# Optimization experiments

Measured on AMD Instinct MI355X. Metric: run time of the kernel, lower is better.

Reference implementation:

```python
import jax, jax.numpy as jnp
import numpy as np

E_PROP = 0.8
DT = 0.02
AX = 0.2   # dt / tau_x = 0.02 / 0.1
AW = 0.02  # dt / tau_w = 0.02 / 1.0


def _ei_mask(out_size, in_size, e_prop, zero_prop, remove_diag):
    """EILinear mask: +1 for excitatory cols, -1 inhibitory, 0 for zeroed cols/diag."""
    e = int(e_prop * in_size)
    sign = np.ones(in_size, np.float32)
    sign[e:] = -1.0
    zc = int(round(zero_prop * in_size))
    exist = np.ones(in_size, np.float32)
    if zc > 0:
        exist[in_size - zc:] = 0.0
    m = np.tile((sign * exist)[None, :], (out_size, 1))
    if remove_diag:
        assert out_size == in_size
        m[np.eye(out_size, dtype=bool)] = 0.0
    return jnp.asarray(m)


def setup_inputs() -> dict:
    T, B, I, H, O = 32, 16, 128, 384, 32
    key = jax.random.key(0)
    ks = jax.random.split(key, 10)
    u = lambda k, s, hi: jax.random.uniform(k, s, jnp.float32, 0.0, hi)
    s_in = (1.0 / I) ** 0.5
    s_h = (1.0 / H) ** 0.5
    s_hz = (1.0 / (H - round((1.0 - E_PROP) * H))) ** 0.5  # zero_cols removed from fan-in
    return {
        "x": jax.random.normal(ks[0], (T, B, I), jnp.float32),
        "Rs": jax.random.uniform(ks[1], (T, B, 1), jnp.float32),
        "W_x2c": u(ks[2], (H, I), 0.5 * s_in),
        "W_c2c": u(ks[3], (H, H), s_h),
        "b_c2c": jnp.zeros((H,), jnp.float32),
        "W_c2h": u(ks[4], (H, H), 0.5 * s_hz),
        "W_h2h": u(ks[5], (H, H), s_h),
        "b_h2h": jnp.zeros((H,), jnp.float32),
        "W_h2o": u(ks[6], (O, H), 0.5 * s_hz),
        "W_attn": u(ks[7], (H, H), 0.1 * s_hz),
        "b_attn": jnp.zeros((H,), jnp.float32),
        "kappa": jnp.full((12,), AW, jnp.float32),
    }


def reference(x, Rs, W_x2c, W_c2c, b_c2c, W_c2h, W_h2h, b_h2h, W_h2o, W_attn, b_attn, kappa):
    T, B, I = x.shape
    H = W_c2c.shape[0]
    O = W_h2o.shape[0]
    retanh = lambda z: jnp.tanh(jax.nn.relu(z))

    m_x2c = _ei_mask(H, I, 1.0, 0.0, False)
    m_c2c = _ei_mask(H, H, E_PROP, 0.0, True)
    m_c2h = _ei_mask(H, H, 1.0, 1.0 - E_PROP, False)
    m_h2h = _ei_mask(H, H, E_PROP, 0.0, True)
    m_h2o = _ei_mask(O, H, 1.0, 1.0 - E_PROP, False)
    m_attn = _ei_mask(H, H, E_PROP, 1.0 - E_PROP, False)

    def plin(W, mask, w_fast, inp, bias=None):
        # (relu(W) + w_fast) * mask, per-batch matmul: [B,O,I] @ [B,I] -> [B,O]
        eff = (jax.nn.relu(W)[None] + w_fast) * mask[None]
        out = jnp.einsum('boi,bi->bo', eff, inp)
        return out if bias is None else out + bias

    def lin(W, mask, inp, bias=None):
        out = inp @ (jax.nn.relu(W) * mask).T
        return out if bias is None else out + bias

    def plast(w, R, pre, post, k, W_slow):
        # w: [B,O,I]; R: [B,1,1]; pre: [B,I]; post: [B,O]
        new_w = (w * (1.0 - AW)
                 + DT * R * (k[0] * pre[:, None, :]
                             + k[1] * post[:, :, None]
                             + k[2] * post[:, :, None] * pre[:, None, :]))
        lb = -jax.lax.stop_gradient(jax.nn.relu(W_slow))[None]
        return jnp.maximum(new_w, lb)

    def step(carry, inputs):
        x_t, R_t = inputs  # [B,I], [B,1]
        sc, oc, sh, oh, wxc, wcc, wch, whh = carry
        attn = retanh(lin(W_attn, m_attn, oh, b_attn))  # attention_type == 'bias'
        tic = plin(W_x2c, m_x2c, wxc, x_t) + plin(W_c2c, m_c2c, wcc, oc, b_c2c) + attn
        nsc = sc * (1.0 - AX) + tic * AX
        noc = retanh(nsc)
        tih = plin(W_c2h, m_c2h, wch, noc) + plin(W_h2h, m_h2h, whh, oh, b_h2h)
        nsh = sh * (1.0 - AX) + tih * AX
        noh = retanh(nsh)
        R = R_t[:, :, None]  # [B,1,1]
        wxc2 = plast(wxc, R, x_t, noc, kappa[0:3], W_x2c)
        wcc2 = plast(wcc, R, oc, noc, kappa[3:6], W_c2c)
        wch2 = plast(wch, R, noc, noh, kappa[6:9], W_c2h)
        whh2 = plast(whh, R, oh, noh, kappa[9:12], W_h2h)
        out_t = lin(W_h2o, m_h2o, noh)
        return (nsc, noc, nsh, noh, wxc2, wcc2, wch2, whh2), out_t

    z = jnp.zeros((B, H), x.dtype)
    carry0 = (z, z, z, z,
              jnp.zeros((B, H, I), x.dtype),
              jnp.zeros((B, H, H), x.dtype),
              jnp.zeros((B, H, H), x.dtype),
              jnp.zeros((B, H, H), x.dtype))
    _, outs = jax.lax.scan(step, carry0, (x, Rs))
    return outs  # [T, B, O]
```

## Files before the change

### kernel.cpp

```cpp
#include <hip/hip_runtime.h>


#define NT 32
#define NBATCH 16
#define DI 128
#define DH 384
#define DOUT 32
#define CSZ (NT * NBATCH * DH)

__device__ __forceinline__ float retanh_f(float z) {
  z = fmaxf(z, 0.0f);
  float e = __expf(-2.0f * z);
  return (1.0f - e) / (1.0f + e);
}

__device__ __forceinline__ float aldf(const float* p) {
  return __hip_atomic_load(p, __ATOMIC_RELAXED, __HIP_MEMORY_SCOPE_AGENT);
}
__device__ __forceinline__ void pubG(float* p, float v) {
  __hip_atomic_store(p, v, __ATOMIC_RELAXED, __HIP_MEMORY_SCOPE_AGENT);
}

__device__ __forceinline__ void gather6G(const float* src, int lane, float arr[6]) {
  const float* p = src + lane;
  float v0, v1, v2, v3, v4, v5;
  for (;;) {
    v0 = aldf(p + 0 * 64);
    v1 = aldf(p + 1 * 64);
    v2 = aldf(p + 2 * 64);
    v3 = aldf(p + 3 * 64);
    v4 = aldf(p + 4 * 64);
    v5 = aldf(p + 5 * 64);
    const bool ok = (v0 != 0.f) & (v1 != 0.f) & (v2 != 0.f) &
                    (v3 != 0.f) & (v4 != 0.f) & (v5 != 0.f);
    if (ok) break;
  }
  arr[0] = v0 - 2.f; arr[1] = v1 - 2.f; arr[2] = v2 - 2.f;
  arr[3] = v3 - 2.f; arr[4] = v4 - 2.f; arr[5] = v5 - 2.f;
}

__global__ __launch_bounds__(512, 2) void hrnn(
    const float* __restrict__ x, const float* __restrict__ Rs,
    const float* __restrict__ Wx, const float* __restrict__ Wc, const float* __restrict__ bc,
    const float* __restrict__ Wch, const float* __restrict__ Whh, const float* __restrict__ bh,
    const float* __restrict__ Wo, const float* __restrict__ Wa, const float* __restrict__ ba,
    const float* __restrict__ kap, float* __restrict__ out, float* __restrict__ comm) {
  const int tid  = threadIdx.x;
  const int lane = tid & 63;
  const int wv   = tid >> 6;
  const int bid  = blockIdx.x;
  const int b = ((bid & 7) << 1) | ((bid >> 3) & 1);
  const int k = bid >> 4;

  float* noc_buf = comm;
  float* noh_buf = comm + CSZ;

  __shared__ float sh_noh[DH];
  __shared__ float sh_noc[DH];

  const int og0 = k * 24 + wv * 3;
  const bool do_out = (k == 15);

  float wxc[3][2], wcc[3][6], wchv[3][5], whh[3][6];
  float rWx[3][2], rWc[3][6], rWch[3][5], rWhh[3][6], rWa[3][5];
  float sc[3], shs[3], bcr[3], bar[3], bhr[3];
  float ohr[6], ocr[6];
  float rWo[4][5];

#pragma unroll
  for (int r = 0; r < 3; ++r) {
    const int og = og0 + r;
#pragma unroll
    for (int j = 0; j < 2; ++j) { rWx[r][j] = fmaxf(Wx[og*DI + j*64 + lane], 0.f); wxc[r][j] = 0.f; }
#pragma unroll
    for (int j = 0; j < 6; ++j) { rWc[r][j] = fmaxf(Wc[og*DH + j*64 + lane], 0.f); wcc[r][j] = 0.f; }
#pragma unroll
    for (int j = 0; j < 5; ++j) { rWch[r][j] = fmaxf(Wch[og*DH + j*64 + lane], 0.f); wchv[r][j] = 0.f; }
#pragma unroll
    for (int j = 0; j < 6; ++j) { rWhh[r][j] = fmaxf(Whh[og*DH + j*64 + lane], 0.f); whh[r][j] = 0.f; }
#pragma unroll
    for (int j = 0; j < 5; ++j) {
      float w = fmaxf(Wa[og*DH + j*64 + lane], 0.f);
      rWa[r][j] = (j == 4 && lane >= 51) ? 0.f : w;
    }
    sc[r] = 0.f; shs[r] = 0.f;
    bcr[r] = bc[og]; bar[r] = ba[og]; bhr[r] = bh[og];
  }
  if (do_out) {
#pragma unroll
    for (int m = 0; m < 4; ++m) {
      const int o = wv * 4 + m;
#pragma unroll
      for (int j = 0; j < 5; ++j) {
        float w = fmaxf(Wo[o*DH + j*64 + lane], 0.f);
        rWo[m][j] = (j == 4 && lane >= 51) ? 0.f : w;
      }
    }
  }
#pragma unroll
  for (int j = 0; j < 6; ++j) { ohr[j] = 0.f; ocr[j] = 0.f; }
  float kp[12];
#pragma unroll
  for (int j = 0; j < 12; ++j) kp[j] = kap[j];

  float xp0 = x[b*DI + lane];
  float xp1 = x[b*DI + 64 + lane];
  float dtRp = 0.02f * Rs[b];

  for (int t = 0; t < NT; ++t) {
    const int toff = t * NBATCH * DH + b * DH;

    if (t > 0) {
      if (wv == 0) {
        float tmp[6];
        gather6G(noh_buf + toff - NBATCH * DH, lane, tmp);
#pragma unroll
        for (int j = 0; j < 6; ++j) sh_noh[j * 64 + lane] = tmp[j];
      }
      __syncthreads();
#pragma unroll
      for (int j = 0; j < 6; ++j) ohr[j] = sh_noh[j * 64 + lane];
    }

    const float dtR = dtRp;
    const float x0 = xp0;
    const float x1 = xp1;
    const float oh4s = (lane < 51) ? ohr[4] : -ohr[4];
    const float oc4s = (lane < 51) ? ocr[4] : -ocr[4];
    const float inC[6] = { ocr[0], ocr[1], ocr[2], ocr[3], oc4s, -ocr[5] };

    float nocr[3];
#pragma unroll
    for (int r = 0; r < 3; ++r) {
      const int og = og0 + r;
      const int dj = og >> 6, dl = og & 63;
      float accA = 0.f, accT = 0.f;
#pragma unroll
      for (int j = 0; j < 5; ++j) accA += rWa[r][j] * ohr[j];
      accT += (rWx[r][0] + wxc[r][0]) * x0;
      accT += (rWx[r][1] + wxc[r][1]) * x1;
#pragma unroll
      for (int j = 0; j < 6; ++j) {
        float term = (rWc[r][j] + wcc[r][j]) * inC[j];
        if (j == dj) term = (lane == dl) ? 0.f : term;
        accT += term;
      }
#pragma unroll
      for (int mm = 1; mm <= 32; mm <<= 1) {
        accA += __shfl_xor(accA, mm, 64);
        accT += __shfl_xor(accT, mm, 64);
      }
      const float attn = retanh_f(accA + bar[r]);
      const float tic = accT + bcr[r] + attn;
      sc[r] = 0.8f*sc[r] + 0.2f*tic;
      nocr[r] = retanh_f(sc[r]);
    }
    {
      float mine = (lane == 0) ? nocr[0] : (lane == 1) ? nocr[1] : nocr[2];
      if (lane < 3) pubG(noc_buf + toff + og0 + lane, mine + 2.0f);
    }

    if (t < NT-1) {
      xp0 = x[((t+1)*NBATCH + b)*DI + lane];
      xp1 = x[((t+1)*NBATCH + b)*DI + 64 + lane];
      dtRp = 0.02f * Rs[(t+1)*NBATCH + b];
    }
    if (do_out && t > 0) {
#pragma unroll
      for (int m = 0; m < 4; ++m) {
        float a = 0.f;
#pragma unroll
        for (int j = 0; j < 5; ++j) a += rWo[m][j] * ohr[j];
#pragma unroll
        for (int mm = 1; mm <= 32; mm <<= 1) a += __shfl_xor(a, mm, 64);
        if (lane == 0) out[(t-1)*NBATCH*DOUT + b*DOUT + wv*4 + m] = a;
      }
    }
    if (t < NT-1) {
      float axc[2], bxc[2];
#pragma unroll
      for (int j = 0; j < 2; ++j) {
        const float pre = (j == 0) ? x0 : x1;
        axc[j] = dtR*kp[0]*pre; bxc[j] = dtR*(kp[1] + kp[2]*pre);
      }
      float acc_[6], bcc_[6];
#pragma unroll
      for (int j = 0; j < 6; ++j) { acc_[j] = dtR*kp[3]*ocr[j]; bcc_[j] = dtR*(kp[4] + kp[5]*ocr[j]); }
#pragma unroll
      for (int r = 0; r < 3; ++r) {
        const float post = nocr[r];
#pragma unroll
        for (int j = 0; j < 2; ++j)
          wxc[r][j] = fmaxf(fmaf(wxc[r][j], 0.98f, fmaf(bxc[j], post, axc[j])), -rWx[r][j]);
#pragma unroll
        for (int j = 0; j < 6; ++j)
          wcc[r][j] = fmaxf(fmaf(wcc[r][j], 0.98f, fmaf(bcc_[j], post, acc_[j])), -rWc[r][j]);
      }
    }

    if (wv == 0) {
      float tmp[6];
      gather6G(noc_buf + toff, lane, tmp);
#pragma unroll
      for (int j = 0; j < 6; ++j) sh_noc[j * 64 + lane] = tmp[j];
    }
    __syncthreads();
    float ncr[6];
#pragma unroll
    for (int j = 0; j < 6; ++j) ncr[j] = sh_noc[j * 64 + lane];

    const float nc4z = (lane < 51) ? ncr[4] : 0.f;
    const float inH[6] = { ohr[0], ohr[1], ohr[2], ohr[3], oh4s, -ohr[5] };
    const float inN[5] = { ncr[0], ncr[1], ncr[2], ncr[3], nc4z };
    float nohr[3];
#pragma unroll
    for (int r = 0; r < 3; ++r) {
      const int og = og0 + r;
      const int dj = og >> 6, dl = og & 63;
      float acc = 0.f;
#pragma unroll
      for (int j = 0; j < 5; ++j) acc += (rWch[r][j] + wchv[r][j]) * inN[j];
#pragma unroll
      for (int j = 0; j < 6; ++j) {
        float term = (rWhh[r][j] + whh[r][j]) * inH[j];
        if (j == dj) term = (lane == dl) ? 0.f : term;
        acc += term;
      }
#pragma unroll
      for (int mm = 1; mm <= 32; mm <<= 1) acc += __shfl_xor(acc, mm, 64);
      const float tih = acc + bhr[r];
      shs[r] = 0.8f*shs[r] + 0.2f*tih;
      nohr[r] = retanh_f(shs[r]);
    }
    {
      float mine = (lane == 0) ? nohr[0] : (lane == 1) ? nohr[1] : nohr[2];
      if (lane < 3) pubG(noh_buf + toff + og0 + lane, mine + 2.0f);
    }

    if (t < NT-1) {
      float an_[5], bn_[5];
#pragma unroll
      for (int j = 0; j < 5; ++j) { an_[j] = dtR*kp[6]*ncr[j]; bn_[j] = dtR*(kp[7] + kp[8]*ncr[j]); }
      float ah_[6], bh_[6];
#pragma unroll
      for (int j = 0; j < 6; ++j) { ah_[j] = dtR*kp[9]*ohr[j]; bh_[j] = dtR*(kp[10] + kp[11]*ohr[j]); }
#pragma unroll
      for (int r = 0; r < 3; ++r) {
        const float post = nohr[r];
#pragma unroll
        for (int j = 0; j < 5; ++j)
          wchv[r][j] = fmaxf(fmaf(wchv[r][j], 0.98f, fmaf(bn_[j], post, an_[j])), -rWch[r][j]);
#pragma unroll
        for (int j = 0; j < 6; ++j)
          whh[r][j] = fmaxf(fmaf(whh[r][j], 0.98f, fmaf(bh_[j], post, ah_[j])), -rWhh[r][j]);
      }
    }
#pragma unroll
    for (int j = 0; j < 6; ++j) ocr[j] = ncr[j];
  }

  if (do_out) {
    if (wv == 0) {
      float tmp[6];
      gather6G(noh_buf + (NT-1)*NBATCH*DH + b*DH, lane, tmp);
#pragma unroll
      for (int j = 0; j < 6; ++j) sh_noh[j * 64 + lane] = tmp[j];
    }
    __syncthreads();
    float oh2[6];
#pragma unroll
    for (int j = 0; j < 6; ++j) oh2[j] = sh_noh[j * 64 + lane];
#pragma unroll
    for (int m = 0; m < 4; ++m) {
      float a = 0.f;
#pragma unroll
      for (int j = 0; j < 5; ++j) a += rWo[m][j] * oh2[j];
#pragma unroll
      for (int mm = 1; mm <= 32; mm <<= 1) a += __shfl_xor(a, mm, 64);
      if (lane == 0) out[(NT-1)*NBATCH*DOUT + b*DOUT + wv*4 + m] = a;
    }
  }
}

extern "C" void kernel_launch(void* const* d_in, const int* in_sizes, int n_in,
                              void* d_out, int out_size, void* d_ws, size_t ws_size,
                              hipStream_t stream) {
  const float* x   = (const float*)d_in[0];
  const float* Rs  = (const float*)d_in[1];
  const float* Wx  = (const float*)d_in[2];
  const float* Wc  = (const float*)d_in[3];
  const float* bc  = (const float*)d_in[4];
  const float* Wch = (const float*)d_in[5];
  const float* Whh = (const float*)d_in[6];
  const float* bh  = (const float*)d_in[7];
  const float* Wo  = (const float*)d_in[8];
  const float* Wa  = (const float*)d_in[9];
  const float* ba  = (const float*)d_in[10];
  const float* kap = (const float*)d_in[11];
  float* out = (float*)d_out;

  float* comm = (float*)d_ws;
  hipMemsetAsync(comm, 0, (size_t)2 * CSZ * sizeof(float), stream);

  hipLaunchKernelGGL(hrnn, dim3(256), dim3(512), 0, stream,
                     x, Rs, Wx, Wc, bc, Wch, Whh, bh, Wo, Wa, ba, kap,
                     out, comm);
}
```

Before: 170.0 us.

## Split compute and polling waves, with dedicated poller waves filling shared state

Each block of 8 waves now has 6 compute waves handling 4 rows each, plus two dedicated waves that poll the cross-block noc and noh buffers and fill shared memory. Before, the compute waves did this themselves. The aim is to overlap the global spin-gather with the compute waves' plasticity updates and to keep polling off the compute waves' critical path. Output-projection weights are no longer held in registers; they are reloaded from global memory each step, which lowers register pressure at the cost of extra loads. Each compute wave now carries more register state, and the block still synchronises twice per step.

```diff
diff --git a/kernel.cpp b/kernel.cpp
--- a/kernel.cpp
+++ b/kernel.cpp
@@ -58,226 +58,225 @@
   __shared__ float sh_noh[DH];
   __shared__ float sh_noc[DH];
 
-  const int og0 = k * 24 + wv * 3;
-  const bool do_out = (k == 15);
-
-  float wxc[3][2], wcc[3][6], wchv[3][5], whh[3][6];
-  float rWx[3][2], rWc[3][6], rWch[3][5], rWhh[3][6], rWa[3][5];
-  float sc[3], shs[3], bcr[3], bar[3], bhr[3];
+  const bool is_cw    = (wv < 6);
+  const bool is_pollC = (wv == 6);
+  const bool is_pollH = (wv == 7);
+  const int  og0 = k * 24 + wv * 4;
+  const bool do_out = (k == 15) && is_cw;
+
+  float wxc[4][2], wcc[4][6], wchv[4][5], whh[4][6];
+  float rWx[4][2], rWc[4][6], rWch[4][5], rWhh[4][6], rWa[4][5];
+  float sc[4], shs[4], bcr[4], bar4[4], bhr[4];
   float ohr[6], ocr[6];
-  float rWo[4][5];
-
-#pragma unroll
-  for (int r = 0; r < 3; ++r) {
-    const int og = og0 + r;
-#pragma unroll
-    for (int j = 0; j < 2; ++j) { rWx[r][j] = fmaxf(Wx[og*DI + j*64 + lane], 0.f); wxc[r][j] = 0.f; }
-#pragma unroll
-    for (int j = 0; j < 6; ++j) { rWc[r][j] = fmaxf(Wc[og*DH + j*64 + lane], 0.f); wcc[r][j] = 0.f; }
-#pragma unroll
-    for (int j = 0; j < 5; ++j) { rWch[r][j] = fmaxf(Wch[og*DH + j*64 + lane], 0.f); wchv[r][j] = 0.f; }
-#pragma unroll
-    for (int j = 0; j < 6; ++j) { rWhh[r][j] = fmaxf(Whh[og*DH + j*64 + lane], 0.f); whh[r][j] = 0.f; }
-#pragma unroll
-    for (int j = 0; j < 5; ++j) {
-      float w = fmaxf(Wa[og*DH + j*64 + lane], 0.f);
-      rWa[r][j] = (j == 4 && lane >= 51) ? 0.f : w;
+  float kp[12];
+  float xp0 = 0.f, xp1 = 0.f, dtRp = 0.f;
+
+  if (is_cw) {
+#pragma unroll
+    for (int r = 0; r < 4; ++r) {
+      const int og = og0 + r;
+#pragma unroll
+      for (int j = 0; j < 2; ++j) { rWx[r][j] = fmaxf(Wx[og*DI + j*64 + lane], 0.f); wxc[r][j] = 0.f; }
+#pragma unroll
+      for (int j = 0; j < 6; ++j) { rWc[r][j] = fmaxf(Wc[og*DH + j*64 + lane], 0.f); wcc[r][j] = 0.f; }
+#pragma unroll
+      for (int j = 0; j < 5; ++j) { rWch[r][j] = fmaxf(Wch[og*DH + j*64 + lane], 0.f); wchv[r][j] = 0.f; }
+#pragma unroll
+      for (int j = 0; j < 6; ++j) { rWhh[r][j] = fmaxf(Whh[og*DH + j*64 + lane], 0.f); whh[r][j] = 0.f; }
+#pragma unroll
+      for (int j = 0; j < 5; ++j) {
+        float w = fmaxf(Wa[og*DH + j*64 + lane], 0.f);
+        rWa[r][j] = (j == 4 && lane >= 51) ? 0.f : w;
+      }
+      sc[r] = 0.f; shs[r] = 0.f;
+      bcr[r] = bc[og]; bar4[r] = ba[og]; bhr[r] = bh[og];
     }
-    sc[r] = 0.f; shs[r] = 0.f;
-    bcr[r] = bc[og]; bar[r] = ba[og]; bhr[r] = bh[og];
+#pragma unroll
+    for (int j = 0; j < 12; ++j) kp[j] = kap[j];
+    xp0 = x[b*DI + lane];
+    xp1 = x[b*DI + 64 + lane];
+    dtRp = 0.02f * Rs[b];
   }
-  if (do_out) {
-#pragma unroll
-    for (int m = 0; m < 4; ++m) {
-      const int o = wv * 4 + m;
-#pragma unroll
-      for (int j = 0; j < 5; ++j) {
-        float w = fmaxf(Wo[o*DH + j*64 + lane], 0.f);
-        rWo[m][j] = (j == 4 && lane >= 51) ? 0.f : w;
-      }
+#pragma unroll
+  for (int j = 0; j < 6; ++j) { ohr[j] = 0.f; ocr[j] = 0.f; }
+
+  for (int t = 0; t < NT; ++t) {
+    const int toff = t * NBATCH * DH + b * DH;
+
+    __syncthreads();
+    if (is_cw) {
+      if (t > 0) {
+#pragma unroll
+        for (int j = 0; j < 6; ++j) ohr[j] = sh_noh[j * 64 + lane];
+      }
+      const float dtR = dtRp;
+      const float x0 = xp0;
+      const float x1 = xp1;
+      const float oc4s = (lane < 51) ? ocr[4] : -ocr[4];
+      const float inC[6] = { ocr[0], ocr[1], ocr[2], ocr[3], oc4s, -ocr[5] };
+      float nocr[4];
+#pragma unroll
+      for (int r = 0; r < 4; ++r) {
+        const int og = og0 + r;
+        const int dj = og >> 6, dl = og & 63;
+        float accA = 0.f, accT = 0.f;
+#pragma unroll
+        for (int j = 0; j < 5; ++j) accA += rWa[r][j] * ohr[j];
+        accT += (rWx[r][0] + wxc[r][0]) * x0;
+        accT += (rWx[r][1] + wxc[r][1]) * x1;
+#pragma unroll
+        for (int j = 0; j < 6; ++j) {
+          float term = (rWc[r][j] + wcc[r][j]) * inC[j];
+          if (j == dj) term = (lane == dl) ? 0.f : term;
+          accT += term;
+        }
+#pragma unroll
+        for (int mm = 1; mm <= 32; mm <<= 1) {
+          accA += __shfl_xor(accA, mm, 64);
+          accT += __shfl_xor(accT, mm, 64);
+        }
+        const float attn = retanh_f(accA + bar4[r]);
+        const float tic = accT + bcr[r] + attn;
+        sc[r] = 0.8f*sc[r] + 0.2f*tic;
+        nocr[r] = retanh_f(sc[r]);
+      }
+      {
+        float mine = (lane == 0) ? nocr[0] : (lane == 1) ? nocr[1]
+                   : (lane == 2) ? nocr[2] : nocr[3];
+        if (lane < 4) pubG(noc_buf + toff + og0 + lane, mine + 2.0f);
+      }
+      if (t < NT-1) {
+        float axc[2], bxc[2];
+#pragma unroll
+        for (int j = 0; j < 2; ++j) {
+          const float pre = (j == 0) ? x0 : x1;
+          axc[j] = dtR*kp[0]*pre; bxc[j] = dtR*(kp[1] + kp[2]*pre);
+        }
+        float acc_[6], bcc_[6];
+#pragma unroll
+        for (int j = 0; j < 6; ++j) { acc_[j] = dtR*kp[3]*ocr[j]; bcc_[j] = dtR*(kp[4] + kp[5]*ocr[j]); }
+#pragma unroll
+        for (int r = 0; r < 4; ++r) {
+          const float post = nocr[r];
+#pragma unroll
+          for (int j = 0; j < 2; ++j)
+            wxc[r][j] = fmaxf(fmaf(wxc[r][j], 0.98f, fmaf(bxc[j], post, axc[j])), -rWx[r][j]);
+#pragma unroll
+          for (int j = 0; j < 6; ++j)
+            wcc[r][j] = fmaxf(fmaf(wcc[r][j], 0.98f, fmaf(bcc_[j], post, acc_[j])), -rWc[r][j]);
+        }
+      }
+      if (do_out && t > 0) {
+#pragma unroll
+        for (int m = 0; m < 6; ++m) {
+          const int row = wv + 6 * m;
+          if (row < DOUT) {
+            float a = 0.f;
+#pragma unroll
+            for (int j = 0; j < 5; ++j) {
+              float w = fmaxf(Wo[row*DH + j*64 + lane], 0.f);
+              if (j == 4 && lane >= 51) w = 0.f;
+              a += w * ohr[j];
+            }
+#pragma unroll
+            for (int mm = 1; mm <= 32; mm <<= 1) a += __shfl_xor(a, mm, 64);
+            if (lane == 0) out[(t-1)*NBATCH*DOUT + b*DOUT + row] = a;
+          }
+        }
+      }
+    } else if (is_pollC) {
+      float tmp[6];
+      gather6G(noc_buf + toff, lane, tmp);
+#pragma unroll
+      for (int j = 0; j < 6; ++j) sh_noc[j * 64 + lane] = tmp[j];
+    }
+
+    __syncthreads();
+    if (is_cw) {
+      float ncr[6];
+#pragma unroll
+      for (int j = 0; j < 6; ++j) ncr[j] = sh_noc[j * 64 + lane];
+      const float dtR = dtRp;
+      const float nc4z = (lane < 51) ? ncr[4] : 0.f;
+      const float oh4s = (lane < 51) ? ohr[4] : -ohr[4];
+      const float inH[6] = { ohr[0], ohr[1], ohr[2], ohr[3], oh4s, -ohr[5] };
+      const float inN[5] = { ncr[0], ncr[1], ncr[2], ncr[3], nc4z };
+      float nohr[4];
+#pragma unroll
+      for (int r = 0; r < 4; ++r) {
+        const int og = og0 + r;
+        const int dj = og >> 6, dl = og & 63;
+        float acc = 0.f;
+#pragma unroll
+        for (int j = 0; j < 5; ++j) acc += (rWch[r][j] + wchv[r][j]) * inN[j];
+#pragma unroll
+        for (int j = 0; j < 6; ++j) {
+          float term = (rWhh[r][j] + whh[r][j]) * inH[j];
+          if (j == dj) term = (lane == dl) ? 0.f : term;
+          acc += term;
+        }
+#pragma unroll
+        for (int mm = 1; mm <= 32; mm <<= 1) acc += __shfl_xor(acc, mm, 64);
+        const float tih = acc + bhr[r];
+        shs[r] = 0.8f*shs[r] + 0.2f*tih;
+        nohr[r] = retanh_f(shs[r]);
+      }
+      {
+        float mine = (lane == 0) ? nohr[0] : (lane == 1) ? nohr[1]
+                   : (lane == 2) ? nohr[2] : nohr[3];
+        if (lane < 4) pubG(noh_buf + toff + og0 + lane, mine + 2.0f);
+      }
+      if (t < NT-1) {
+        float an_[5], bn_[5];
+#pragma unroll
+        for (int j = 0; j < 5; ++j) { an_[j] = dtR*kp[6]*ncr[j]; bn_[j] = dtR*(kp[7] + kp[8]*ncr[j]); }
+        float ah_[6], bh_[6];
+#pragma unroll
+        for (int j = 0; j < 6; ++j) { ah_[j] = dtR*kp[9]*ohr[j]; bh_[j] = dtR*(kp[10] + kp[11]*ohr[j]); }
+#pragma unroll
+        for (int r = 0; r < 4; ++r) {
+          const float post = nohr[r];
+#pragma unroll
+          for (int j = 0; j < 5; ++j)
+            wchv[r][j] = fmaxf(fmaf(wchv[r][j], 0.98f, fmaf(bn_[j], post, an_[j])), -rWch[r][j]);
+#pragma unroll
+          for (int j = 0; j < 6; ++j)
+            whh[r][j] = fmaxf(fmaf(whh[r][j], 0.98f, fmaf(bh_[j], post, ah_[j])), -rWhh[r][j]);
+        }
+        xp0 = x[((t+1)*NBATCH + b)*DI + lane];
+        xp1 = x[((t+1)*NBATCH + b)*DI + 64 + lane];
+        dtRp = 0.02f * Rs[(t+1)*NBATCH + b];
+      }
+#pragma unroll
+      for (int j = 0; j < 6; ++j) ocr[j] = ncr[j];
+    } else if (is_pollH) {
+      float tmp[6];
+      gather6G(noh_buf + toff, lane, tmp);
+#pragma unroll
+      for (int j = 0; j < 6; ++j) sh_noh[j * 64 + lane] = tmp[j];
     }
   }
-#pragma unroll
-  for (int j = 0; j < 6; ++j) { ohr[j] = 0.f; ocr[j] = 0.f; }
-  float kp[12];
-#pragma unroll
-  for (int j = 0; j < 12; ++j) kp[j] = kap[j];
-
-  float xp0 = x[b*DI + lane];
-  float xp1 = x[b*DI + 64 + lane];
-  float dtRp = 0.02f * Rs[b];
-
-  for (int t = 0; t < NT; ++t) {
-    const int toff = t * NBATCH * DH + b * DH;
-
-    if (t > 0) {
-      if (wv == 0) {
-        float tmp[6];
-        gather6G(noh_buf + toff - NBATCH * DH, lane, tmp);
-#pragma unroll
-        for (int j = 0; j < 6; ++j) sh_noh[j * 64 + lane] = tmp[j];
-      }
-      __syncthreads();
-#pragma unroll
-      for (int j = 0; j < 6; ++j) ohr[j] = sh_noh[j * 64 + lane];
-    }
-
-    const float dtR = dtRp;
-    const float x0 = xp0;
-    const float x1 = xp1;
-    const float oh4s = (lane < 51) ? ohr[4] : -ohr[4];
-    const float oc4s = (lane < 51) ? ocr[4] : -ocr[4];
-    const float inC[6] = { ocr[0], ocr[1], ocr[2], ocr[3], oc4s, -ocr[5] };
-
-    float nocr[3];
-#pragma unroll
-    for (int r = 0; r < 3; ++r) {
-      const int og = og0 + r;
-      const int dj = og >> 6, dl = og & 63;
-      float accA = 0.f, accT = 0.f;
-#pragma unroll
-      for (int j = 0; j < 5; ++j) accA += rWa[r][j] * ohr[j];
-      accT += (rWx[r][0] + wxc[r][0]) * x0;
-      accT += (rWx[r][1] + wxc[r][1]) * x1;
-#pragma unroll
-      for (int j = 0; j < 6; ++j) {
-        float term = (rWc[r][j] + wcc[r][j]) * inC[j];
-        if (j == dj) term = (lane == dl) ? 0.f : term;
-        accT += term;
-      }
-#pragma unroll
-      for (int mm = 1; mm <= 32; mm <<= 1) {
-        accA += __shfl_xor(accA, mm, 64);
-        accT += __shfl_xor(accT, mm, 64);
-      }
-      const float attn = retanh_f(accA + bar[r]);
-      const float tic = accT + bcr[r] + attn;
-      sc[r] = 0.8f*sc[r] + 0.2f*tic;
-      nocr[r] = retanh_f(sc[r]);
-    }
-    {
-      float mine = (lane == 0) ? nocr[0] : (lane == 1) ? nocr[1] : nocr[2];
-      if (lane < 3) pubG(noc_buf + toff + og0 + lane, mine + 2.0f);
-    }
-
-    if (t < NT-1) {
-      xp0 = x[((t+1)*NBATCH + b)*DI + lane];
-      xp1 = x[((t+1)*NBATCH + b)*DI + 64 + lane];
-      dtRp = 0.02f * Rs[(t+1)*NBATCH + b];
-    }
-    if (do_out && t > 0) {
-#pragma unroll
-      for (int m = 0; m < 4; ++m) {
+
+  __syncthreads();
+  if (do_out) {
+    float oh2[6];
+#pragma unroll
+    for (int j = 0; j < 6; ++j) oh2[j] = sh_noh[j * 64 + lane];
+#pragma unroll
+    for (int m = 0; m < 6; ++m) {
+      const int row = wv + 6 * m;
+      if (row < DOUT) {
         float a = 0.f;
 #pragma unroll
-        for (int j = 0; j < 5; ++j) a += rWo[m][j] * ohr[j];
+        for (int j = 0; j < 5; ++j) {
+          float w = fmaxf(Wo[row*DH + j*64 + lane], 0.f);
+          if (j == 4 && lane >= 51) w = 0.f;
+          a += w * oh2[j];
+        }
 #pragma unroll
         for (int mm = 1; mm <= 32; mm <<= 1) a += __shfl_xor(a, mm, 64);
-        if (lane == 0) out[(t-1)*NBATCH*DOUT + b*DOUT + wv*4 + m] = a;
-      }
-    }
-    if (t < NT-1) {
-      float axc[2], bxc[2];
-#pragma unroll
-      for (int j = 0; j < 2; ++j) {
-        const float pre = (j == 0) ? x0 : x1;
-        axc[j] = dtR*kp[0]*pre; bxc[j] = dtR*(kp[1] + kp[2]*pre);
-      }
-      float acc_[6], bcc_[6];
-#pragma unroll
-      for (int j = 0; j < 6; ++j) { acc_[j] = dtR*kp[3]*ocr[j]; bcc_[j] = dtR*(kp[4] + kp[5]*ocr[j]); }
-#pragma unroll
-      for (int r = 0; r < 3; ++r) {
-        const float post = nocr[r];
-#pragma unroll
-        for (int j = 0; j < 2; ++j)
-          wxc[r][j] = fmaxf(fmaf(wxc[r][j], 0.98f, fmaf(bxc[j], post, axc[j])), -rWx[r][j]);
-#pragma unroll
-        for (int j = 0; j < 6; ++j)
-          wcc[r][j] = fmaxf(fmaf(wcc[r][j], 0.98f, fmaf(bcc_[j], post, acc_[j])), -rWc[r][j]);
-      }
-    }
-
-    if (wv == 0) {
-      float tmp[6];
-      gather6G(noc_buf + toff, lane, tmp);
-#pragma unroll
-      for (int j = 0; j < 6; ++j) sh_noc[j * 64 + lane] = tmp[j];
-    }
-    __syncthreads();
-    float ncr[6];
-#pragma unroll
-    for (int j = 0; j < 6; ++j) ncr[j] = sh_noc[j * 64 + lane];
-
-    const float nc4z = (lane < 51) ? ncr[4] : 0.f;
-    const float inH[6] = { ohr[0], ohr[1], ohr[2], ohr[3], oh4s, -ohr[5] };
-    const float inN[5] = { ncr[0], ncr[1], ncr[2], ncr[3], nc4z };
-    float nohr[3];
-#pragma unroll
-    for (int r = 0; r < 3; ++r) {
-      const int og = og0 + r;
-      const int dj = og >> 6, dl = og & 63;
-      float acc = 0.f;
-#pragma unroll
-      for (int j = 0; j < 5; ++j) acc += (rWch[r][j] + wchv[r][j]) * inN[j];
-#pragma unroll
-      for (int j = 0; j < 6; ++j) {
-        float term = (rWhh[r][j] + whh[r][j]) * inH[j];
-        if (j == dj) term = (lane == dl) ? 0.f : term;
-        acc += term;
-      }
-#pragma unroll
-      for (int mm = 1; mm <= 32; mm <<= 1) acc += __shfl_xor(acc, mm, 64);
-      const float tih = acc + bhr[r];
-      shs[r] = 0.8f*shs[r] + 0.2f*tih;
-      nohr[r] = retanh_f(shs[r]);
-    }
-    {
-      float mine = (lane == 0) ? nohr[0] : (lane == 1) ? nohr[1] : nohr[2];
-      if (lane < 3) pubG(noh_buf + toff + og0 + lane, mine + 2.0f);
-    }
-
-    if (t < NT-1) {
-      float an_[5], bn_[5];
-#pragma unroll
-      for (int j = 0; j < 5; ++j) { an_[j] = dtR*kp[6]*ncr[j]; bn_[j] = dtR*(kp[7] + kp[8]*ncr[j]); }
-      float ah_[6], bh_[6];
-#pragma unroll
-      for (int j = 0; j < 6; ++j) { ah_[j] = dtR*kp[9]*ohr[j]; bh_[j] = dtR*(kp[10] + kp[11]*ohr[j]); }
-#pragma unroll
-      for (int r = 0; r < 3; ++r) {
-        const float post = nohr[r];
-#pragma unroll
-        for (int j = 0; j < 5; ++j)
-          wchv[r][j] = fmaxf(fmaf(wchv[r][j], 0.98f, fmaf(bn_[j], post, an_[j])), -rWch[r][j]);
-#pragma unroll
-        for (int j = 0; j < 6; ++j)
-          whh[r][j] = fmaxf(fmaf(whh[r][j], 0.98f, fmaf(bh_[j], post, ah_[j])), -rWhh[r][j]);
-      }
-    }
-#pragma unroll
-    for (int j = 0; j < 6; ++j) ocr[j] = ncr[j];
-  }
-
-  if (do_out) {
-    if (wv == 0) {
-      float tmp[6];
-      gather6G(noh_buf + (NT-1)*NBATCH*DH + b*DH, lane, tmp);
-#pragma unroll
-      for (int j = 0; j < 6; ++j) sh_noh[j * 64 + lane] = tmp[j];
-    }
-    __syncthreads();
-    float oh2[6];
-#pragma unroll
-    for (int j = 0; j < 6; ++j) oh2[j] = sh_noh[j * 64 + lane];
-#pragma unroll
-    for (int m = 0; m < 4; ++m) {
-      float a = 0.f;
-#pragma unroll
-      for (int j = 0; j < 5; ++j) a += rWo[m][j] * oh2[j];
-#pragma unroll
-      for (int mm = 1; mm <= 32; mm <<= 1) a += __shfl_xor(a, mm, 64);
-      if (lane == 0) out[(NT-1)*NBATCH*DOUT + b*DOUT + wv*4 + m] = a;
+        if (lane == 0) out[(NT-1)*NBATCH*DOUT + b*DOUT + row] = a;
+      }
     }
   }
 }
```

After: 391.9 us. 2.31x slower.

## Add dedicated polling wavefronts so compute waves skip cross-block gather

Applied to the files above, without the earlier changes.

Grows each block from 8 to 10 wavefronts. Two new wavefronts do nothing but spin on the global noc and noh exchange buffers and stage the results into shared memory. Compute wavefronts no longer run the gather themselves, and the loop is rearranged so the noh poll for the next step runs while the compute waves finish the plasticity updates. This costs more threads per block and a changed launch bound (640, 3), which may constrain register allocation. The extra spinning wave per phase also consumes issue slots.

```diff
diff --git a/kernel.cpp b/kernel.cpp
--- a/kernel.cpp
+++ b/kernel.cpp
@@ -39,7 +39,7 @@
   arr[3] = v3 - 2.f; arr[4] = v4 - 2.f; arr[5] = v5 - 2.f;
 }
 
-__global__ __launch_bounds__(512, 2) void hrnn(
+__global__ __launch_bounds__(640, 3) void hrnn(
     const float* __restrict__ x, const float* __restrict__ Rs,
     const float* __restrict__ Wx, const float* __restrict__ Wc, const float* __restrict__ bc,
     const float* __restrict__ Wch, const float* __restrict__ Whh, const float* __restrict__ bh,
@@ -58,33 +58,45 @@
   __shared__ float sh_noh[DH];
   __shared__ float sh_noc[DH];
 
-  const int og0 = k * 24 + wv * 3;
-  const bool do_out = (k == 15);
+  const bool is_cw    = (wv < 8);
+  const bool is_pollC = (wv == 8);
+  const bool is_pollH = (wv == 9);
+  const int  og0 = k * 24 + wv * 3;
+  const bool do_out = (k == 15) && is_cw;
 
   float wxc[3][2], wcc[3][6], wchv[3][5], whh[3][6];
   float rWx[3][2], rWc[3][6], rWch[3][5], rWhh[3][6], rWa[3][5];
-  float sc[3], shs[3], bcr[3], bar[3], bhr[3];
+  float sc[3], shs[3], bcr[3], bar3[3], bhr[3];
   float ohr[6], ocr[6];
   float rWo[4][5];
-
-#pragma unroll
-  for (int r = 0; r < 3; ++r) {
-    const int og = og0 + r;
-#pragma unroll
-    for (int j = 0; j < 2; ++j) { rWx[r][j] = fmaxf(Wx[og*DI + j*64 + lane], 0.f); wxc[r][j] = 0.f; }
-#pragma unroll
-    for (int j = 0; j < 6; ++j) { rWc[r][j] = fmaxf(Wc[og*DH + j*64 + lane], 0.f); wcc[r][j] = 0.f; }
-#pragma unroll
-    for (int j = 0; j < 5; ++j) { rWch[r][j] = fmaxf(Wch[og*DH + j*64 + lane], 0.f); wchv[r][j] = 0.f; }
-#pragma unroll
-    for (int j = 0; j < 6; ++j) { rWhh[r][j] = fmaxf(Whh[og*DH + j*64 + lane], 0.f); whh[r][j] = 0.f; }
-#pragma unroll
-    for (int j = 0; j < 5; ++j) {
-      float w = fmaxf(Wa[og*DH + j*64 + lane], 0.f);
-      rWa[r][j] = (j == 4 && lane >= 51) ? 0.f : w;
-    }
-    sc[r] = 0.f; shs[r] = 0.f;
-    bcr[r] = bc[og]; bar[r] = ba[og]; bhr[r] = bh[og];
+  float kp[12];
+  float xp0 = 0.f, xp1 = 0.f, dtRp = 0.f;
+
+  if (is_cw) {
+#pragma unroll
+    for (int r = 0; r < 3; ++r) {
+      const int og = og0 + r;
+#pragma unroll
+      for (int j = 0; j < 2; ++j) { rWx[r][j] = fmaxf(Wx[og*DI + j*64 + lane], 0.f); wxc[r][j] = 0.f; }
+#pragma unroll
+      for (int j = 0; j < 6; ++j) { rWc[r][j] = fmaxf(Wc[og*DH + j*64 + lane], 0.f); wcc[r][j] = 0.f; }
+#pragma unroll
+      for (int j = 0; j < 5; ++j) { rWch[r][j] = fmaxf(Wch[og*DH + j*64 + lane], 0.f); wchv[r][j] = 0.f; }
+#pragma unroll
+      for (int j = 0; j < 6; ++j) { rWhh[r][j] = fmaxf(Whh[og*DH + j*64 + lane], 0.f); whh[r][j] = 0.f; }
+#pragma unroll
+      for (int j = 0; j < 5; ++j) {
+        float w = fmaxf(Wa[og*DH + j*64 + lane], 0.f);
+        rWa[r][j] = (j == 4 && lane >= 51) ? 0.f : w;
+      }
+      sc[r] = 0.f; shs[r] = 0.f;
+      bcr[r] = bc[og]; bar3[r] = ba[og]; bhr[r] = bh[og];
+    }
+#pragma unroll
+    for (int j = 0; j < 12; ++j) kp[j] = kap[j];
+    xp0 = x[b*DI + lane];
+    xp1 = x[b*DI + 64 + lane];
+    dtRp = 0.02f * Rs[b];
   }
   if (do_out) {
 #pragma unroll
@@ -99,174 +111,157 @@
   }
 #pragma unroll
   for (int j = 0; j < 6; ++j) { ohr[j] = 0.f; ocr[j] = 0.f; }
-  float kp[12];
-#pragma unroll
-  for (int j = 0; j < 12; ++j) kp[j] = kap[j];
-
-  float xp0 = x[b*DI + lane];
-  float xp1 = x[b*DI + 64 + lane];
-  float dtRp = 0.02f * Rs[b];
 
   for (int t = 0; t < NT; ++t) {
     const int toff = t * NBATCH * DH + b * DH;
 
-    if (t > 0) {
-      if (wv == 0) {
-        float tmp[6];
-        gather6G(noh_buf + toff - NBATCH * DH, lane, tmp);
-#pragma unroll
-        for (int j = 0; j < 6; ++j) sh_noh[j * 64 + lane] = tmp[j];
-      }
-      __syncthreads();
-#pragma unroll
-      for (int j = 0; j < 6; ++j) ohr[j] = sh_noh[j * 64 + lane];
-    }
-
-    const float dtR = dtRp;
-    const float x0 = xp0;
-    const float x1 = xp1;
-    const float oh4s = (lane < 51) ? ohr[4] : -ohr[4];
-    const float oc4s = (lane < 51) ? ocr[4] : -ocr[4];
-    const float inC[6] = { ocr[0], ocr[1], ocr[2], ocr[3], oc4s, -ocr[5] };
-
-    float nocr[3];
-#pragma unroll
-    for (int r = 0; r < 3; ++r) {
-      const int og = og0 + r;
-      const int dj = og >> 6, dl = og & 63;
-      float accA = 0.f, accT = 0.f;
-#pragma unroll
-      for (int j = 0; j < 5; ++j) accA += rWa[r][j] * ohr[j];
-      accT += (rWx[r][0] + wxc[r][0]) * x0;
-      accT += (rWx[r][1] + wxc[r][1]) * x1;
-#pragma unroll
-      for (int j = 0; j < 6; ++j) {
-        float term = (rWc[r][j] + wcc[r][j]) * inC[j];
-        if (j == dj) term = (lane == dl) ? 0.f : term;
-        accT += term;
-      }
-#pragma unroll
-      for (int mm = 1; mm <= 32; mm <<= 1) {
-        accA += __shfl_xor(accA, mm, 64);
-        accT += __shfl_xor(accT, mm, 64);
-      }
-      const float attn = retanh_f(accA + bar[r]);
-      const float tic = accT + bcr[r] + attn;
-      sc[r] = 0.8f*sc[r] + 0.2f*tic;
-      nocr[r] = retanh_f(sc[r]);
-    }
-    {
-      float mine = (lane == 0) ? nocr[0] : (lane == 1) ? nocr[1] : nocr[2];
-      if (lane < 3) pubG(noc_buf + toff + og0 + lane, mine + 2.0f);
-    }
-
-    if (t < NT-1) {
-      xp0 = x[((t+1)*NBATCH + b)*DI + lane];
-      xp1 = x[((t+1)*NBATCH + b)*DI + 64 + lane];
-      dtRp = 0.02f * Rs[(t+1)*NBATCH + b];
-    }
-    if (do_out && t > 0) {
-#pragma unroll
-      for (int m = 0; m < 4; ++m) {
-        float a = 0.f;
-#pragma unroll
-        for (int j = 0; j < 5; ++j) a += rWo[m][j] * ohr[j];
-#pragma unroll
-        for (int mm = 1; mm <= 32; mm <<= 1) a += __shfl_xor(a, mm, 64);
-        if (lane == 0) out[(t-1)*NBATCH*DOUT + b*DOUT + wv*4 + m] = a;
-      }
-    }
-    if (t < NT-1) {
-      float axc[2], bxc[2];
-#pragma unroll
-      for (int j = 0; j < 2; ++j) {
-        const float pre = (j == 0) ? x0 : x1;
-        axc[j] = dtR*kp[0]*pre; bxc[j] = dtR*(kp[1] + kp[2]*pre);
-      }
-      float acc_[6], bcc_[6];
-#pragma unroll
-      for (int j = 0; j < 6; ++j) { acc_[j] = dtR*kp[3]*ocr[j]; bcc_[j] = dtR*(kp[4] + kp[5]*ocr[j]); }
+    __syncthreads();
+    if (is_cw) {
+      if (t > 0) {
+#pragma unroll
+        for (int j = 0; j < 6; ++j) ohr[j] = sh_noh[j * 64 + lane];
+      }
+      const float dtR = dtRp;
+      const float x0 = xp0;
+      const float x1 = xp1;
+      const float oc4s = (lane < 51) ? ocr[4] : -ocr[4];
+      const float inC[6] = { ocr[0], ocr[1], ocr[2], ocr[3], oc4s, -ocr[5] };
+      float nocr[3];
 #pragma unroll
       for (int r = 0; r < 3; ++r) {
-        const float post = nocr[r];
-#pragma unroll
-        for (int j = 0; j < 2; ++j)
-          wxc[r][j] = fmaxf(fmaf(wxc[r][j], 0.98f, fmaf(bxc[j], post, axc[j])), -rWx[r][j]);
-#pragma unroll
-        for (int j = 0; j < 6; ++j)
-          wcc[r][j] = fmaxf(fmaf(wcc[r][j], 0.98f, fmaf(bcc_[j], post, acc_[j])), -rWc[r][j]);
-      }
-    }
-
-    if (wv == 0) {
+        const int og = og0 + r;
+        const int dj = og >> 6, dl = og & 63;
+        float accA = 0.f, accT = 0.f;
+#pragma unroll
+        for (int j = 0; j < 5; ++j) accA += rWa[r][j] * ohr[j];
+        accT += (rWx[r][0] + wxc[r][0]) * x0;
+        accT += (rWx[r][1] + wxc[r][1]) * x1;
+#pragma unroll
+        for (int j = 0; j < 6; ++j) {
+          float term = (rWc[r][j] + wcc[r][j]) * inC[j];
+          if (j == dj) term = (lane == dl) ? 0.f : term;
+          accT += term;
+        }
+#pragma unroll
+        for (int mm = 1; mm <= 32; mm <<= 1) {
+          accA += __shfl_xor(accA, mm, 64);
+          accT += __shfl_xor(accT, mm, 64);
+        }
+        const float attn = retanh_f(accA + bar3[r]);
+        const float tic = accT + bcr[r] + attn;
+        sc[r] = 0.8f*sc[r] + 0.2f*tic;
+        nocr[r] = retanh_f(sc[r]);
+      }
+      {
+        float mine = (lane == 0) ? nocr[0] : (lane == 1) ? nocr[1] : nocr[2];
+        if (lane < 3) pubG(noc_buf + toff + og0 + lane, mine + 2.0f);
+      }
+      if (t < NT-1) {
+        float axc[2], bxc[2];
+#pragma unroll
+        for (int j = 0; j < 2; ++j) {
+          const float pre = (j == 0) ? x0 : x1;
+          axc[j] = dtR*kp[0]*pre; bxc[j] = dtR*(kp[1] + kp[2]*pre);
+        }
+        float acc_[6], bcc_[6];
+#pragma unroll
+        for (int j = 0; j < 6; ++j) { acc_[j] = dtR*kp[3]*ocr[j]; bcc_[j] = dtR*(kp[4] + kp[5]*ocr[j]); }
+#pragma unroll
+        for (int r = 0; r < 3; ++r) {
+          const float post = nocr[r];
+#pragma unroll
+          for (int j = 0; j < 2; ++j)
+            wxc[r][j] = fmaxf(fmaf(wxc[r][j], 0.98f, fmaf(bxc[j], post, axc[j])), -rWx[r][j]);
+#pragma unroll
+          for (int j = 0; j < 6; ++j)
+            wcc[r][j] = fmaxf(fmaf(wcc[r][j], 0.98f, fmaf(bcc_[j], post, acc_[j])), -rWc[r][j]);
+        }
+      }
+      if (do_out && t > 0) {
+#pragma unroll
+        for (int m = 0; m < 4; ++m) {
+          float a = 0.f;
+#pragma unroll
+          for (int j = 0; j < 5; ++j) a += rWo[m][j] * ohr[j];
+#pragma unroll
+          for (int mm = 1; mm <= 32; mm <<= 1) a += __shfl_xor(a, mm, 64);
+          if (lane == 0) out[(t-1)*NBATCH*DOUT + b*DOUT + wv*4 + m] = a;
+        }
+      }
+    } else if (is_pollC) {
       float tmp[6];
       gather6G(noc_buf + toff, lane, tmp);
 #pragma unroll
       for (int j = 0; j < 6; ++j) sh_noc[j * 64 + lane] = tmp[j];
     }
+
     __syncthreads();
-    float ncr[6];
-#pragma unroll
-    for (int j = 0; j < 6; ++j) ncr[j] = sh_noc[j * 64 + lane];
-
-    const float nc4z = (lane < 51) ? ncr[4] : 0.f;
-    const float inH[6] = { ohr[0], ohr[1], ohr[2], ohr[3], oh4s, -ohr[5] };
-    const float inN[5] = { ncr[0], ncr[1], ncr[2], ncr[3], nc4z };
-    float nohr[3];
-#pragma unroll
-    for (int r = 0; r < 3; ++r) {
-      const int og = og0 + r;
-      const int dj = og >> 6, dl = og & 63;
-      float acc = 0.f;
-#pragma unroll
-      for (int j = 0; j < 5; ++j) acc += (rWch[r][j] + wchv[r][j]) * inN[j];
-#pragma unroll
-      for (int j = 0; j < 6; ++j) {
-        float term = (rWhh[r][j] + whh[r][j]) * inH[j];
-        if (j == dj) term = (lane == dl) ? 0.f : term;
-        acc += term;
-      }
-#pragma unroll
-      for (int mm = 1; mm <= 32; mm <<= 1) acc += __shfl_xor(acc, mm, 64);
-      const float tih = acc + bhr[r];
-      shs[r] = 0.8f*shs[r] + 0.2f*tih;
-      nohr[r] = retanh_f(shs[r]);
-    }
-    {
-      float mine = (lane == 0) ? nohr[0] : (lane == 1) ? nohr[1] : nohr[2];
-      if (lane < 3) pubG(noh_buf + toff + og0 + lane, mine + 2.0f);
-    }
-
-    if (t < NT-1) {
-      float an_[5], bn_[5];
-#pragma unroll
-      for (int j = 0; j < 5; ++j) { an_[j] = dtR*kp[6]*ncr[j]; bn_[j] = dtR*(kp[7] + kp[8]*ncr[j]); }
-      float ah_[6], bh_[6];
-#pragma unroll
-      for (int j = 0; j < 6; ++j) { ah_[j] = dtR*kp[9]*ohr[j]; bh_[j] = dtR*(kp[10] + kp[11]*ohr[j]); }
+    if (is_cw) {
+      float ncr[6];
+#pragma unroll
+      for (int j = 0; j < 6; ++j) ncr[j] = sh_noc[j * 64 + lane];
+      const float dtR = dtRp;
+      const float nc4z = (lane < 51) ? ncr[4] : 0.f;
+      const float oh4s = (lane < 51) ? ohr[4] : -ohr[4];
+      const float inH[6] = { ohr[0], ohr[1], ohr[2], ohr[3], oh4s, -ohr[5] };
+      const float inN[5] = { ncr[0], ncr[1], ncr[2], ncr[3], nc4z };
+      float nohr[3];
 #pragma unroll
       for (int r = 0; r < 3; ++r) {
-        const float post = nohr[r];
-#pragma unroll
-        for (int j = 0; j < 5; ++j)
-          wchv[r][j] = fmaxf(fmaf(wchv[r][j], 0.98f, fmaf(bn_[j], post, an_[j])), -rWch[r][j]);
-#pragma unroll
-        for (int j = 0; j < 6; ++j)
-          whh[r][j] = fmaxf(fmaf(whh[r][j], 0.98f, fmaf(bh_[j], post, ah_[j])), -rWhh[r][j]);
-      }
-    }
-#pragma unroll
-    for (int j = 0; j < 6; ++j) ocr[j] = ncr[j];
-  }
-
+        const int og = og0 + r;
+        const int dj = og >> 6, dl = og & 63;
+        float acc = 0.f;
+#pragma unroll
+        for (int j = 0; j < 5; ++j) acc += (rWch[r][j] + wchv[r][j]) * inN[j];
+#pragma unroll
+        for (int j = 0; j < 6; ++j) {
+          float term = (rWhh[r][j] + whh[r][j]) * inH[j];
+          if (j == dj) term = (lane == dl) ? 0.f : term;
+          acc += term;
+        }
+#pragma unroll
+        for (int mm = 1; mm <= 32; mm <<= 1) acc += __shfl_xor(acc, mm, 64);
+        const float tih = acc + bhr[r];
+        shs[r] = 0.8f*shs[r] + 0.2f*tih;
+        nohr[r] = retanh_f(shs[r]);
+      }
+      {
+        float mine = (lane == 0) ? nohr[0] : (lane == 1) ? nohr[1] : nohr[2];
+        if (lane < 3) pubG(noh_buf + toff + og0 + lane, mine + 2.0f);
+      }
+      if (t < NT-1) {
+        float an_[5], bn_[5];
+#pragma unroll
+        for (int j = 0; j < 5; ++j) { an_[j] = dtR*kp[6]*ncr[j]; bn_[j] = dtR*(kp[7] + kp[8]*ncr[j]); }
+        float ah_[6], bh_[6];
+#pragma unroll
+        for (int j = 0; j < 6; ++j) { ah_[j] = dtR*kp[9]*ohr[j]; bh_[j] = dtR*(kp[10] + kp[11]*ohr[j]); }
+#pragma unroll
+        for (int r = 0; r < 3; ++r) {
+          const float post = nohr[r];
+#pragma unroll
+          for (int j = 0; j < 5; ++j)
+            wchv[r][j] = fmaxf(fmaf(wchv[r][j], 0.98f, fmaf(bn_[j], post, an_[j])), -rWch[r][j]);
+#pragma unroll
+          for (int j = 0; j < 6; ++j)
+            whh[r][j] = fmaxf(fmaf(whh[r][j], 0.98f, fmaf(bh_[j], post, ah_[j])), -rWhh[r][j]);
+        }
+        xp0 = x[((t+1)*NBATCH + b)*DI + lane];
+        xp1 = x[((t+1)*NBATCH + b)*DI + 64 + lane];
+        dtRp = 0.02f * Rs[(t+1)*NBATCH + b];
+      }
+#pragma unroll
+      for (int j = 0; j < 6; ++j) ocr[j] = ncr[j];
+    } else if (is_pollH) {
+      float tmp[6];
+      gather6G(noh_buf + toff, lane, tmp);
+#pragma unroll
+      for (int j = 0; j < 6; ++j) sh_noh[j * 64 + lane] = tmp[j];
+    }
+  }
+
+  __syncthreads();
   if (do_out) {
-    if (wv == 0) {
-      float tmp[6];
-      gather6G(noh_buf + (NT-1)*NBATCH*DH + b*DH, lane, tmp);
-#pragma unroll
-      for (int j = 0; j < 6; ++j) sh_noh[j * 64 + lane] = tmp[j];
-    }
-    __syncthreads();
     float oh2[6];
 #pragma unroll
     for (int j = 0; j < 6; ++j) oh2[j] = sh_noh[j * 64 + lane];
@@ -302,7 +297,7 @@
   float* comm = (float*)d_ws;
   hipMemsetAsync(comm, 0, (size_t)2 * CSZ * sizeof(float), stream);
 
-  hipLaunchKernelGGL(hrnn, dim3(256), dim3(512), 0, stream,
+  hipLaunchKernelGGL(hrnn, dim3(256), dim3(640), 0, stream,
                      x, Rs, Wx, Wc, bc, Wch, Whh, bh, Wo, Wa, ba, kap,
                      out, comm);
 }
```

After: 582.0 us. 242% more time.
